# Kernel optimization log

Hardware: AMD Instinct MI355X
Metric: run time of the kernel (lower is better)

## Reference

```python
import jax, jax.numpy as jnp
import numpy as np

N = 50000      # nodes
E = 800000     # edges (avg degree 16)
F_IN = 128
H = 128        # hidden_channels
C = 10         # num_classes
S = 5          # Chebyshev order K
B = 8          # graphs in batch


def setup_inputs() -> dict:
    key = jax.random.key(0)
    ks = jax.random.split(key, 9)
    x = jax.random.normal(ks[0], (N, F_IN), jnp.float32)
    edge_index = jax.random.randint(ks[1], (2, E), 0, N, dtype=jnp.int64)
    batch = jnp.sort(jax.random.randint(ks[2], (N,), 0, B, dtype=jnp.int64))
    lambda_max = 2.0 * jnp.ones((B,), jnp.float32)
    W1 = jax.random.normal(ks[3], (S, F_IN, H), jnp.float32) * 0.05
    b1 = jax.random.normal(ks[4], (H,), jnp.float32) * 0.05
    W2 = jax.random.normal(ks[5], (S, H, H), jnp.float32) * 0.05
    b2 = jax.random.normal(ks[6], (H,), jnp.float32) * 0.05
    Wlin = jax.random.normal(ks[7], (H, C), jnp.float32) * 0.05
    blin = jax.random.normal(ks[8], (C,), jnp.float32) * 0.05
    return {"x": x, "edge_index": edge_index, "batch": batch,
            "lambda_max": lambda_max, "W1": W1, "b1": b1,
            "W2": W2, "b2": b2, "Wlin": Wlin, "blin": blin}


def _cheb_conv(x, row, col, w_edge, diag, W, b):
    # scaled Laplacian matvec: L_hat v = scatter(w_edge * v[col] -> row) + diag * v
    def Lhat(v):
        msg = v[col] * w_edge[:, None]                       # [E, d]
        return jax.ops.segment_sum(msg, row, num_segments=N) + diag[:, None] * v

    Tx0 = x
    out = Tx0 @ W[0]
    Tx1 = Lhat(Tx0)
    out = out + Tx1 @ W[1]
    for k in range(2, W.shape[0]):                           # Chebyshev recurrence
        Tx2 = 2.0 * Lhat(Tx1) - Tx0
        out = out + Tx2 @ W[k]
        Tx0, Tx1 = Tx1, Tx2
    return out + b


def reference(x, edge_index, batch, lambda_max, W1, b1, W2, b2, Wlin, blin):
    row, col = edge_index[0], edge_index[1]
    # sym-normalized Laplacian L = I - D^{-1/2} A D^{-1/2}; L_hat = 2L/lambda_max - I
    deg = jax.ops.segment_sum(jnp.ones((E,), x.dtype), row, num_segments=N)
    dis = jnp.where(deg > 0, jax.lax.rsqrt(jnp.maximum(deg, 1e-12)), 0.0)
    lam_e = lambda_max[batch[row]]                           # per-edge lambda_max
    w_edge = -2.0 * dis[row] * dis[col] / lam_e              # off-diagonal of L_hat
    diag = 2.0 / lambda_max[batch] - 1.0                     # diagonal of L_hat per node

    h = jax.nn.relu(_cheb_conv(x, row, col, w_edge, diag, W1, b1))
    h = jax.nn.relu(_cheb_conv(h, row, col, w_edge, diag, W2, b2))

    # global_mean_pool over batch assignment
    sums = jax.ops.segment_sum(h, batch, num_segments=B)     # [B, H]
    counts = jax.ops.segment_sum(jnp.ones((N, 1), h.dtype), batch, num_segments=B)
    pooled = sums / jnp.maximum(counts, 1.0)
    return pooled @ Wlin + blin                              # [B, C] logits (softmax unused in forward)
```

## Files before the change

### kernel.cpp

```cpp
#include <hip/hip_runtime.h>
#include <hip/hip_bf16.h>
#include <stdint.h>

typedef __attribute__((ext_vector_type(8))) short bf16x8;
typedef __attribute__((ext_vector_type(4))) float f32x4;

__device__ __forceinline__ float bf16lo_to_f(uint32_t u) { return __uint_as_float(u << 16); }
__device__ __forceinline__ float bf16hi_to_f(uint32_t u) { return __uint_as_float(u & 0xffff0000u); }
__device__ __forceinline__ uint16_t f_to_bf16(float f) {
    uint32_t u = __float_as_uint(f);
    uint32_t r = u + 0x7fff + ((u >> 16) & 1);
    return (uint16_t)(r >> 16);
}


#define BINCH 4096

__global__ void __launch_bounds__(256) k_bhist(const int* __restrict__ row,
                                               int* __restrict__ bhist, int E) {
    __shared__ int sh[256];
    int t = threadIdx.x;
    sh[t] = 0;
    __syncthreads();
    int stride = gridDim.x * blockDim.x;
    for (int e = blockIdx.x * blockDim.x + t; e < E; e += stride)
        atomicAdd(&sh[row[e] >> 8], 1);
    __syncthreads();
    if (sh[t]) atomicAdd(&bhist[t], sh[t]);
}

__global__ void k_bscan(const int* __restrict__ bhist, int* __restrict__ gbase,
                        int* __restrict__ gcur, float* __restrict__ mS, int nbk, int N) {
    __shared__ int sh[256];
    int t = threadIdx.x;
    int v = t < nbk ? bhist[t] : 0;
    sh[t] = v;
    __syncthreads();
    for (int o = 1; o < 256; o <<= 1) {
        int u = (t >= o) ? sh[t - o] : 0;
        __syncthreads();
        sh[t] += u;
        __syncthreads();
    }
    gbase[t] = sh[t] - v;
    gcur[t] = sh[t] - v;
    if (t == 255) gbase[256] = sh[255];
    if (t < 5) mS[(size_t)t * (N + 1) + N] = 0.f;
}

__global__ void __launch_bounds__(256) k_bin(const int* __restrict__ row,
        const int* __restrict__ col, int* __restrict__ gcur,
        uint32_t* __restrict__ bout, int E) {
    __shared__ uint32_t stage[BINCH];
    __shared__ int hist[256], hscan[256], hcur[256], gofs[256];
    int t = threadIdx.x;
    int e0 = blockIdx.x * BINCH;
    int ecnt = min(BINCH, E - e0);
    hist[t] = 0;
    __syncthreads();
    for (int i = t; i < ecnt; i += 256)
        atomicAdd(&hist[row[e0 + i] >> 8], 1);
    __syncthreads();
    int v = hist[t];
    hscan[t] = v;
    __syncthreads();
    for (int o = 1; o < 256; o <<= 1) {
        int u = (t >= o) ? hscan[t - o] : 0;
        __syncthreads();
        hscan[t] += u;
        __syncthreads();
    }
    hcur[t] = hscan[t] - v;
    __syncthreads();
    for (int i = t; i < ecnt; i += 256) {
        int r = row[e0 + i];
        int p = atomicAdd(&hcur[r >> 8], 1);
        stage[p] = (uint32_t)(r & 255) | ((uint32_t)col[e0 + i] << 8);
    }
    __syncthreads();
    if (v > 0) gofs[t] = atomicAdd(&gcur[t], v);
    __syncthreads();
    for (int i = t; i < ecnt; i += 256) {
        int lo = 0, hi = 255;
        while (lo < hi) { int mid = (lo + hi) >> 1; if (hscan[mid] > i) hi = mid; else lo = mid + 1; }
        int b = lo;
        int local = i - (hscan[b] - hist[b]);
        bout[gofs[b] + local] = stage[i];
    }
}

__global__ void __launch_bounds__(256) k_deg2(const uint32_t* __restrict__ bout,
        const int* __restrict__ gbase, int* __restrict__ deg,
        int* __restrict__ psum, int N) {
    __shared__ int cnt[256];
    __shared__ int red[256];
    int t = threadIdx.x, b = blockIdx.x;
    cnt[t] = 0;
    __syncthreads();
    int s = gbase[b], epos = gbase[b + 1];
    for (int i = s + t; i < epos; i += 256)
        atomicAdd(&cnt[bout[i] & 255], 1);
    __syncthreads();
    int n = b * 256 + t;
    int d = cnt[t];
    if (n < N) deg[n] = d;
    red[t] = (n < N) ? ((d + 7) & ~7) : 0;
    __syncthreads();
    for (int o = 128; o > 0; o >>= 1) {
        if (t < o) red[t] += red[t + o];
        __syncthreads();
    }
    if (t == 0) psum[b] = red[0];
}

__global__ void k_offs(const int* __restrict__ deg, const int* __restrict__ psum,
                       int* __restrict__ offs,
                       const int* __restrict__ batch, const float* __restrict__ lam,
                       float* __restrict__ dis, float* __restrict__ diag,
                       int N, int nb) {
    __shared__ int pre[256];
    __shared__ int sh[256];
    int t = threadIdx.x, b = blockIdx.x;
    pre[t] = (t < b) ? psum[t] : 0;
    __syncthreads();
    for (int o = 128; o > 0; o >>= 1) {
        if (t < o) pre[t] += pre[t + o];
        __syncthreads();
    }
    int base = pre[0];
    __syncthreads();
    int idx = b * 256 + t;
    int d = idx < N ? deg[idx] : 0;
    int v = (d + 7) & ~7;
    sh[t] = v;
    __syncthreads();
    for (int o = 1; o < 256; o <<= 1) {
        int u = (t >= o) ? sh[t - o] : 0;
        __syncthreads();
        sh[t] += u;
        __syncthreads();
    }
    if (idx < N) {
        offs[idx] = base + sh[t] - v;
        dis[idx] = d > 0 ? rsqrtf((float)d) : 0.f;
        diag[idx] = 2.f / lam[batch[idx]] - 1.f;
    }
    if (b == nb - 1 && t == 255) offs[N] = base + sh[255];
}

__global__ void __launch_bounds__(256) k_csr2(const uint32_t* __restrict__ bout,
        const int* __restrict__ gbase, const int* __restrict__ offs,
        uint16_t* __restrict__ csr, int N) {
    __shared__ int cur[256];
    int t = threadIdx.x, b = blockIdx.x;
    int n = b * 256 + t;
    int o0 = n < N ? offs[n] : 0;
    cur[t] = o0;
    __syncthreads();
    int s = gbase[b], epos = gbase[b + 1];
    for (int i = s + t; i < epos; i += 256) {
        uint32_t v = bout[i];
        int p = atomicAdd(&cur[v & 255], 1);
        csr[p] = (uint16_t)(v >> 8);
    }
    __syncthreads();
    if (n < N) {
        int e = cur[t];
        int pe = o0 + ((e - o0 + 7) & ~7);
        for (int p = e; p < pe; p++) csr[p] = (uint16_t)N;
    }
}

__global__ void k_prepw(const float* __restrict__ W1, uint16_t* __restrict__ Wt1,
                        const float* __restrict__ W2, uint16_t* __restrict__ Wt2) {
    int i = blockIdx.x * blockDim.x + threadIdx.x;
    const float* W = W1; uint16_t* Wt = Wt1;
    if (i >= 128 * 640) { i -= 128 * 640; W = W2; Wt = Wt2; }
    int o = i / 640, kk = i % 640;
    Wt[(size_t)o * 640 + kk] = f_to_bf16(W[(size_t)kk * 128 + o]);
}

__global__ void __launch_bounds__(256) k_castx(const float* __restrict__ x,
        uint16_t* __restrict__ Txb, int8_t* __restrict__ Txq,
        const float* __restrict__ dis, float* __restrict__ mS,
        float* __restrict__ scq, int N) {
    int n = (blockIdx.x * blockDim.x + threadIdx.x) >> 6;
    int lane = threadIdx.x & 63;
    if (n >= N) return;
    float2 v = ((const float2*)x)[(size_t)n * 64 + lane];
    uint32_t p = (uint32_t)f_to_bf16(v.x) | ((uint32_t)f_to_bf16(v.y) << 16);
    __builtin_nontemporal_store(p, &((uint32_t*)Txb)[(size_t)n * 320 + lane]);
    float m = fmaxf(fabsf(v.x), fabsf(v.y));
    for (int o = 1; o < 64; o <<= 1) m = fmaxf(m, __shfl_xor(m, o));
    float inv = m > 0.f ? 127.f / m : 0.f;
    int qx = (int)rintf(v.x * inv), qy = (int)rintf(v.y * inv);
    uint16_t qp = (uint16_t)((qx & 0xff) | ((qy & 0xff) << 8));
    *(uint16_t*)(Txq + (size_t)n * 640 + 2 * lane) = qp;
    if (lane == 0) {
        float sc = m > 0.f ? m * (1.f / 127.f) : 0.f;
        mS[n] = sc * dis[n];
        scq[n] = sc;
    }
}

__global__ void __launch_bounds__(256) k_lhat(
        int8_t* __restrict__ Txq, uint16_t* __restrict__ Txb,
        const int* __restrict__ offs, const uint16_t* __restrict__ csr,
        const float* __restrict__ diag, const float* __restrict__ dis,
        float* __restrict__ mS, float* __restrict__ scq, int N,
        int src, int dst, int prev, float alpha, int use_prev) {
    int n = (blockIdx.x * blockDim.x + threadIdx.x) >> 6;
    int lane = threadIdx.x & 63;
    if (n >= N) return;
    int beg = offs[n], end = offs[n + 1];
    float dgn = diag[n], dn = dis[n];
    float aS = -alpha * dn * (dgn + 1.0f);
    const float* mSrc = mS + (size_t)src * (N + 1);
    const int8_t* qbase = Txq + src * 128 + 2 * lane;
    float ax = 0.f, ay = 0.f;
    for (int e = beg; e < end; e += 8) {
        uint4 cw = *(const uint4*)(csr + e);
        int cc[8] = { (int)(cw.x & 0xffff), (int)(cw.x >> 16),
                      (int)(cw.y & 0xffff), (int)(cw.y >> 16),
                      (int)(cw.z & 0xffff), (int)(cw.z >> 16),
                      (int)(cw.w & 0xffff), (int)(cw.w >> 16) };
        float mm[8];
        uint16_t qv[8];
#pragma unroll
        for (int u = 0; u < 8; u++) mm[u] = mSrc[cc[u]];
#pragma unroll
        for (int u = 0; u < 8; u++)
            qv[u] = *(const uint16_t*)(qbase + (size_t)cc[u] * 640);
#pragma unroll
        for (int u = 0; u < 8; u++) {
            float f = aS * mm[u];
            ax = fmaf(f, (float)(int)(int8_t)(qv[u] & 0xff), ax);
            ay = fmaf(f, (float)(int)(int8_t)(qv[u] >> 8), ay);
        }
    }
    {
        uint16_t qsv = *(const uint16_t*)(Txq + (size_t)n * 640 + src * 128 + 2 * lane);
        float ad = alpha * dgn * scq[(size_t)src * (N + 1) + n];
        ax = fmaf(ad, (float)(int)(int8_t)(qsv & 0xff), ax);
        ay = fmaf(ad, (float)(int)(int8_t)(qsv >> 8), ay);
    }
    if (use_prev) {
        uint16_t qpv = *(const uint16_t*)(Txq + (size_t)n * 640 + prev * 128 + 2 * lane);
        float sp = scq[(size_t)prev * (N + 1) + n];
        ax = fmaf(-sp, (float)(int)(int8_t)(qpv & 0xff), ax);
        ay = fmaf(-sp, (float)(int)(int8_t)(qpv >> 8), ay);
    }
    uint32_t outv = (uint32_t)f_to_bf16(ax) | ((uint32_t)f_to_bf16(ay) << 16);
    __builtin_nontemporal_store(outv, &((uint32_t*)Txb)[(size_t)n * 320 + dst * 64 + lane]);
    float m = fmaxf(fabsf(ax), fabsf(ay));
    for (int o = 1; o < 64; o <<= 1) m = fmaxf(m, __shfl_xor(m, o));
    float inv = m > 0.f ? 127.f / m : 0.f;
    int qx = (int)rintf(ax * inv), qy = (int)rintf(ay * inv);
    uint16_t qp = (uint16_t)((qx & 0xff) | ((qy & 0xff) << 8));
    *(uint16_t*)(Txq + (size_t)n * 640 + dst * 128 + 2 * lane) = qp;
    if (lane == 0) {
        float sc = m > 0.f ? m * (1.f / 127.f) : 0.f;
        mS[(size_t)dst * (N + 1) + n] = sc * dn;
        scq[(size_t)dst * (N + 1) + n] = sc;
    }
}

#define BM 128
#define BK 64
#define LDT 72
#define LDC 132

__global__ void __launch_bounds__(256) k_gemm(
        const uint16_t* __restrict__ A, int lda,
        const uint16_t* __restrict__ Bt,
        const float* __restrict__ bias,
        uint16_t* __restrict__ out2b,
        int8_t* __restrict__ out2q,
        const float* __restrict__ dis, float* __restrict__ mS,
        float* __restrict__ scq,
        float* __restrict__ pooled,
        const int* __restrict__ batch,
        int M, int Kdim) {
    __shared__ uint16_t smem[BM * LDT + 128 * LDT];
    uint16_t* As = smem;
    uint16_t* Bs = smem + BM * LDT;
    uint16_t* Ct = smem;
    int t = threadIdx.x;
    int w = t >> 6, lane = t & 63;
    int row0 = blockIdx.x * BM;
    int mrow = (w >> 1) * 64, ncol = (w & 1) * 64;

    int ar[4], akc[4];
#pragma unroll
    for (int rep = 0; rep < 4; rep++) {
        int d = rep * 256 + t;
        ar[rep] = d >> 3; akc[rep] = d & 7;
    }

    f32x4 acc[4][4];
#pragma unroll
    for (int i = 0; i < 4; i++)
#pragma unroll
        for (int j = 0; j < 4; j++) acc[i][j] = (f32x4){0.f, 0.f, 0.f, 0.f};

    bf16x8 pa[4], pb[4];
#pragma unroll
    for (int rep = 0; rep < 4; rep++) {
        int grow = row0 + ar[rep];
        bf16x8 va = {0, 0, 0, 0, 0, 0, 0, 0};
        if (grow < M) va = *(const bf16x8*)(A + (size_t)grow * lda + akc[rep] * 8);
        pa[rep] = va;
        pb[rep] = *(const bf16x8*)(Bt + (size_t)ar[rep] * Kdim + akc[rep] * 8);
    }

    for (int k0 = 0; k0 < Kdim; k0 += BK) {
#pragma unroll
        for (int rep = 0; rep < 4; rep++) {
            *(bf16x8*)(&As[ar[rep] * LDT + akc[rep] * 8]) = pa[rep];
            *(bf16x8*)(&Bs[ar[rep] * LDT + akc[rep] * 8]) = pb[rep];
        }
        __syncthreads();
        int kn = k0 + BK;
        if (kn < Kdim) {
#pragma unroll
            for (int rep = 0; rep < 4; rep++) {
                int grow = row0 + ar[rep];
                bf16x8 va = {0, 0, 0, 0, 0, 0, 0, 0};
                if (grow < M) va = *(const bf16x8*)(A + (size_t)grow * lda + kn + akc[rep] * 8);
                pa[rep] = va;
                pb[rep] = *(const bf16x8*)(Bt + (size_t)ar[rep] * Kdim + kn + akc[rep] * 8);
            }
        }
#pragma unroll
        for (int ks = 0; ks < BK; ks += 32) {
            bf16x8 af[4], bfr[4];
#pragma unroll
            for (int i = 0; i < 4; i++) {
                int r = mrow + i * 16 + (lane & 15);
                af[i] = *(const bf16x8*)(&As[r * LDT + ks + (lane >> 4) * 8]);
            }
#pragma unroll
            for (int j = 0; j < 4; j++) {
                int c = ncol + j * 16 + (lane & 15);
                bfr[j] = *(const bf16x8*)(&Bs[c * LDT + ks + (lane >> 4) * 8]);
            }
#pragma unroll
            for (int i = 0; i < 4; i++)
#pragma unroll
                for (int j = 0; j < 4; j++)
                    acc[i][j] = __builtin_amdgcn_mfma_f32_16x16x32_bf16(af[i], bfr[j], acc[i][j], 0, 0, 0);
        }
        __syncthreads();
    }

#pragma unroll
    for (int j = 0; j < 4; j++) {
        int c = ncol + j * 16 + (lane & 15);
        float bv = bias[c];
#pragma unroll
        for (int i = 0; i < 4; i++) {
            int rloc = mrow + i * 16 + (lane >> 4) * 4;
#pragma unroll
            for (int r = 0; r < 4; r++) {
                float v = acc[i][j][r] + bv;
                v = v > 0.f ? v : 0.f;
                Ct[(rloc + r) * LDC + c] = f_to_bf16(v);
            }
        }
    }
    __syncthreads();

    if (out2b) {
#pragma unroll
        for (int rep = 0; rep < 8; rep++) {
            int d = rep * 256 + t;
            int r = d >> 4, c8 = (d & 15) * 8;
            int grow = row0 + r;
            if (grow < M) {
                bf16x8 v = *(const bf16x8*)(&Ct[r * LDC + c8]);
                *(bf16x8*)(out2b + (size_t)grow * 640 + c8) = v;
            }
        }
    }
    if (out2q) {
        int r = t >> 1, half = t & 1;
        int grow = row0 + r;
        float vmax = 0.f;
        for (int j = 0; j < 32; j++) {
            uint32_t u = *(const uint32_t*)(&Ct[r * LDC + half * 64 + j * 2]);
            vmax = fmaxf(vmax, fmaxf(fabsf(bf16lo_to_f(u)), fabsf(bf16hi_to_f(u))));
        }
        vmax = fmaxf(vmax, __shfl_xor(vmax, 1));
        if (grow < M) {
            float inv = vmax > 0.f ? 127.f / vmax : 0.f;
            for (int j0 = 0; j0 < 16; j0++) {
                uint32_t u0 = *(const uint32_t*)(&Ct[r * LDC + half * 64 + j0 * 4]);
                uint32_t u1 = *(const uint32_t*)(&Ct[r * LDC + half * 64 + j0 * 4 + 2]);
                int q0 = (int)rintf(bf16lo_to_f(u0) * inv);
                int q1 = (int)rintf(bf16hi_to_f(u0) * inv);
                int q2 = (int)rintf(bf16lo_to_f(u1) * inv);
                int q3 = (int)rintf(bf16hi_to_f(u1) * inv);
                uint32_t pk = (q0 & 0xff) | ((q1 & 0xff) << 8) |
                              ((q2 & 0xff) << 16) | ((uint32_t)(q3 & 0xff) << 24);
                *(uint32_t*)(out2q + (size_t)grow * 640 + half * 64 + j0 * 4) = pk;
            }
            if (half == 0) {
                float sc = vmax > 0.f ? vmax * (1.f / 127.f) : 0.f;
                mS[grow] = sc * dis[grow];
                scq[grow] = sc;
            }
        }
    }
    if (pooled) {
        int f = t & 127, r0 = (t >> 7) * 64;
        float accp = 0.f;
        int curb = -1;
        for (int r = r0; r < r0 + 64; ++r) {
            int grow = row0 + r;
            if (grow >= M) break;
            int b = batch[grow];
            if (b != curb) {
                if (curb >= 0) atomicAdd(&pooled[curb * 128 + f], accp);
                accp = 0.f; curb = b;
            }
            accp += __uint_as_float(((uint32_t)Ct[r * LDC + f]) << 16);
        }
        if (curb >= 0) atomicAdd(&pooled[curb * 128 + f], accp);
    }
}

__global__ void k_final(const float* __restrict__ pooled, const int* __restrict__ batch,
                        const float* __restrict__ Wlin, const float* __restrict__ blin,
                        float* __restrict__ out, int N, int B_, int C_) {
    __shared__ int cnt[64];
    int t = threadIdx.x;
    if (t < B_) {
        auto lb = [&](int v) {
            int lo = 0, hi = N;
            while (lo < hi) {
                int mid = (lo + hi) >> 1;
                if (batch[mid] < v) lo = mid + 1; else hi = mid;
            }
            return lo;
        };
        cnt[t] = lb(t + 1) - lb(t);
    }
    __syncthreads();
    if (t < B_ * C_) {
        int b = t / C_, c = t % C_;
        float inv = 1.f / fmaxf((float)cnt[b], 1.f);
        float acc = blin[c];
        for (int f = 0; f < 128; ++f) acc += pooled[b * 128 + f] * inv * Wlin[f * C_ + c];
        out[t] = acc;
    }
}

extern "C" void kernel_launch(void* const* d_in, const int* in_sizes, int n_in,
                              void* d_out, int out_size, void* d_ws, size_t ws_size,
                              hipStream_t stream) {
    const float* x    = (const float*)d_in[0];
    const int*   edge = (const int*)d_in[1];
    const int*   batch= (const int*)d_in[2];
    const float* lam  = (const float*)d_in[3];
    const float* W1   = (const float*)d_in[4];
    const float* b1   = (const float*)d_in[5];
    const float* W2   = (const float*)d_in[6];
    const float* b2   = (const float*)d_in[7];
    const float* Wlin = (const float*)d_in[8];
    const float* blin = (const float*)d_in[9];
    const int E  = in_sizes[1] / 2;
    const int N  = in_sizes[2];
    const int B_ = in_sizes[3];
    const int* row = edge;
    const int* col = edge + E;

    char* ws = (char*)d_ws;
    size_t off = 0;
    auto take = [&](size_t bytes) -> char* {
        char* p = ws + off;
        off = (off + bytes + 255) & ~(size_t)255;
        return p;
    };
    uint16_t* Txb    = (uint16_t*)take((size_t)N * 640 * 2);
    int8_t*   Txq    = (int8_t*)take((size_t)(N + 1) * 640);
    uint16_t* csr    = (uint16_t*)take(((size_t)E + 8 * (size_t)N) * 2);
    uint32_t* bout   = (uint32_t*)take((size_t)E * 4);
    float*    mS     = (float*)take((size_t)5 * (N + 1) * 4);
    float*    scq    = (float*)take((size_t)5 * (N + 1) * 4);
    int*      deg    = (int*)take((size_t)N * 4);
    int*      offs   = (int*)take((size_t)(N + 1) * 4);
    float*    dis    = (float*)take((size_t)N * 4);
    float*    diag   = (float*)take((size_t)N * 4);
    uint16_t* Wt1    = (uint16_t*)take((size_t)128 * 640 * 2);
    uint16_t* Wt2    = (uint16_t*)take((size_t)128 * 640 * 2);
    float*    pooled = (float*)take((size_t)B_ * 128 * 4);
    int*      bhist  = (int*)take(257 * 4);
    int*      gbase  = (int*)take(257 * 4);
    int*      gcur   = (int*)take(257 * 4);
    const int nb = (N + 255) / 256;
    int*      psum   = (int*)take((size_t)nb * 4);

    hipMemsetAsync(pooled, 0, (size_t)B_ * 128 * 4 + 257 * 4, stream);

    k_bhist<<<112, 256, 0, stream>>>(row, bhist, E);
    k_bscan<<<1, 256, 0, stream>>>(bhist, gbase, gcur, mS, nb, N);
    k_bin<<<(E + BINCH - 1) / BINCH, 256, 0, stream>>>(row, col, gcur, bout, E);
    k_deg2<<<nb, 256, 0, stream>>>(bout, gbase, deg, psum, N);
    k_offs<<<nb, 256, 0, stream>>>(deg, psum, offs, batch, lam, dis, diag, N, nb);
    k_csr2<<<nb, 256, 0, stream>>>(bout, gbase, offs, csr, N);
    k_prepw<<<(2 * 128 * 640) / 256, 256, 0, stream>>>(W1, Wt1, W2, Wt2);
    k_castx<<<(N + 3) / 4, 256, 0, stream>>>(x, Txb, Txq, dis, mS, scq, N);

    const int lblocks = (N + 3) / 4;
    const int gblocks = (N + BM - 1) / BM;

    k_lhat<<<lblocks, 256, 0, stream>>>(Txq, Txb, offs, csr, diag, dis, mS, scq, N, 0, 1, 0, 1.f, 0);
    k_lhat<<<lblocks, 256, 0, stream>>>(Txq, Txb, offs, csr, diag, dis, mS, scq, N, 1, 2, 0, 2.f, 1);
    k_lhat<<<lblocks, 256, 0, stream>>>(Txq, Txb, offs, csr, diag, dis, mS, scq, N, 2, 3, 1, 2.f, 1);
    k_lhat<<<lblocks, 256, 0, stream>>>(Txq, Txb, offs, csr, diag, dis, mS, scq, N, 3, 4, 2, 2.f, 1);
    k_gemm<<<gblocks, 256, 0, stream>>>(Txb, 640, Wt1, b1,
                                        Txb, Txq, dis, mS, scq,
                                        (float*)nullptr, batch, N, 640);

    k_lhat<<<lblocks, 256, 0, stream>>>(Txq, Txb, offs, csr, diag, dis, mS, scq, N, 0, 1, 0, 1.f, 0);
    k_lhat<<<lblocks, 256, 0, stream>>>(Txq, Txb, offs, csr, diag, dis, mS, scq, N, 1, 2, 0, 2.f, 1);
    k_lhat<<<lblocks, 256, 0, stream>>>(Txq, Txb, offs, csr, diag, dis, mS, scq, N, 2, 3, 1, 2.f, 1);
    k_lhat<<<lblocks, 256, 0, stream>>>(Txq, Txb, offs, csr, diag, dis, mS, scq, N, 3, 4, 2, 2.f, 1);
    k_gemm<<<gblocks, 256, 0, stream>>>(Txb, 640, Wt2, b2,
                                        (uint16_t*)nullptr, (int8_t*)nullptr, dis, mS, scq,
                                        pooled, batch, N, 640);

    k_final<<<1, 128, 0, stream>>>(pooled, batch, Wlin, blin, (float*)d_out, N, B_, 10);
}
```

Before: 482.7 us.

## Replace int8 gather with bf16 stage-major layout and precomputed edge weights

The int8-quantized copies of the Chebyshev terms and their per-row scale arrays are removed. Each stage is now stored as a separate contiguous bf16 plane, with a zero pad row for padding edges. The CSR is rebuilt as 8-byte entries holding a pre-shifted column offset and a precomputed edge weight, so the Lhat kernel drops the per-neighbor scale load and the requantization epilogue. The GEMM now reads A from the stage planes. In exchange, each gathered neighbor row doubles in bytes (bf16 instead of int8) and the edge array grows from 2 to 8 bytes per entry.

```diff
diff --git a/kernel.cpp b/kernel.cpp
--- a/kernel.cpp
+++ b/kernel.cpp
@@ -1,5 +1,4 @@
 #include <hip/hip_runtime.h>
-#include <hip/hip_bf16.h>
 #include <stdint.h>
 
 typedef __attribute__((ext_vector_type(8))) short bf16x8;
@@ -30,7 +29,7 @@
 }
 
 __global__ void k_bscan(const int* __restrict__ bhist, int* __restrict__ gbase,
-                        int* __restrict__ gcur, float* __restrict__ mS, int nbk, int N) {
+                        int* __restrict__ gcur, int nbk) {
     __shared__ int sh[256];
     int t = threadIdx.x;
     int v = t < nbk ? bhist[t] : 0;
@@ -45,7 +44,6 @@
     gbase[t] = sh[t] - v;
     gcur[t] = sh[t] - v;
     if (t == 255) gbase[256] = sh[255];
-    if (t < 5) mS[(size_t)t * (N + 1) + N] = 0.f;
 }
 
 __global__ void __launch_bounds__(256) k_bin(const int* __restrict__ row,
@@ -148,26 +146,33 @@
     if (b == nb - 1 && t == 255) offs[N] = base + sh[255];
 }
 
-__global__ void __launch_bounds__(256) k_csr2(const uint32_t* __restrict__ bout,
+__global__ void __launch_bounds__(256) k_ew(const uint32_t* __restrict__ bout,
         const int* __restrict__ gbase, const int* __restrict__ offs,
-        uint16_t* __restrict__ csr, int N) {
+        const float* __restrict__ dis, const float* __restrict__ diag,
+        uint2* __restrict__ ew, int N) {
     __shared__ int cur[256];
+    __shared__ float srw[256];
     int t = threadIdx.x, b = blockIdx.x;
     int n = b * 256 + t;
     int o0 = n < N ? offs[n] : 0;
     cur[t] = o0;
+    srw[t] = (n < N) ? (-dis[n] * (diag[n] + 1.0f)) : 0.f;
     __syncthreads();
     int s = gbase[b], epos = gbase[b + 1];
     for (int i = s + t; i < epos; i += 256) {
         uint32_t v = bout[i];
-        int p = atomicAdd(&cur[v & 255], 1);
-        csr[p] = (uint16_t)(v >> 8);
+        int r = (int)(v & 255u);
+        int c = (int)(v >> 8);
+        int p = atomicAdd(&cur[r], 1);
+        float w = srw[r] * dis[c];
+        ew[p] = make_uint2((uint32_t)c << 8, __float_as_uint(w));
     }
     __syncthreads();
     if (n < N) {
         int e = cur[t];
         int pe = o0 + ((e - o0 + 7) & ~7);
-        for (int p = e; p < pe; p++) csr[p] = (uint16_t)N;
+        uint2 pad = make_uint2((uint32_t)N << 8, 0u);
+        for (int p = e; p < pe; p++) ew[p] = pad;
     }
 }
 
@@ -181,88 +186,70 @@
 }
 
 __global__ void __launch_bounds__(256) k_castx(const float* __restrict__ x,
-        uint16_t* __restrict__ Txb, int8_t* __restrict__ Txq,
-        const float* __restrict__ dis, float* __restrict__ mS,
-        float* __restrict__ scq, int N) {
+        uint16_t* __restrict__ Txg, int N) {
     int n = (blockIdx.x * blockDim.x + threadIdx.x) >> 6;
     int lane = threadIdx.x & 63;
-    if (n >= N) return;
+    if (n > N) return;
+    size_t ss32 = (size_t)(N + 1) * 64;
+    if (n == N) {
+#pragma unroll
+        for (int s = 0; s < 5; s++)
+            ((uint32_t*)Txg)[s * ss32 + (size_t)N * 64 + lane] = 0u;
+        return;
+    }
     float2 v = ((const float2*)x)[(size_t)n * 64 + lane];
     uint32_t p = (uint32_t)f_to_bf16(v.x) | ((uint32_t)f_to_bf16(v.y) << 16);
-    __builtin_nontemporal_store(p, &((uint32_t*)Txb)[(size_t)n * 320 + lane]);
-    float m = fmaxf(fabsf(v.x), fabsf(v.y));
-    for (int o = 1; o < 64; o <<= 1) m = fmaxf(m, __shfl_xor(m, o));
-    float inv = m > 0.f ? 127.f / m : 0.f;
-    int qx = (int)rintf(v.x * inv), qy = (int)rintf(v.y * inv);
-    uint16_t qp = (uint16_t)((qx & 0xff) | ((qy & 0xff) << 8));
-    *(uint16_t*)(Txq + (size_t)n * 640 + 2 * lane) = qp;
-    if (lane == 0) {
-        float sc = m > 0.f ? m * (1.f / 127.f) : 0.f;
-        mS[n] = sc * dis[n];
-        scq[n] = sc;
-    }
-}
-
-__global__ void __launch_bounds__(256) k_lhat(
-        int8_t* __restrict__ Txq, uint16_t* __restrict__ Txb,
-        const int* __restrict__ offs, const uint16_t* __restrict__ csr,
-        const float* __restrict__ diag, const float* __restrict__ dis,
-        float* __restrict__ mS, float* __restrict__ scq, int N,
+    ((uint32_t*)Txg)[(size_t)n * 64 + lane] = p;
+}
+
+__global__ void __launch_bounds__(256) k_lhat(uint16_t* Txg,
+        const int* __restrict__ offs, const uint2* __restrict__ ew,
+        const float* __restrict__ diag, int N,
         int src, int dst, int prev, float alpha, int use_prev) {
     int n = (blockIdx.x * blockDim.x + threadIdx.x) >> 6;
     int lane = threadIdx.x & 63;
     if (n >= N) return;
     int beg = offs[n], end = offs[n + 1];
-    float dgn = diag[n], dn = dis[n];
-    float aS = -alpha * dn * (dgn + 1.0f);
-    const float* mSrc = mS + (size_t)src * (N + 1);
-    const int8_t* qbase = Txq + src * 128 + 2 * lane;
+    size_t sb = (size_t)(N + 1) * 256;
+    const uint8_t* srcs = (const uint8_t*)Txg + (size_t)src * sb;
+    uint32_t lo4 = (uint32_t)lane * 4;
     float ax = 0.f, ay = 0.f;
     for (int e = beg; e < end; e += 8) {
-        uint4 cw = *(const uint4*)(csr + e);
-        int cc[8] = { (int)(cw.x & 0xffff), (int)(cw.x >> 16),
-                      (int)(cw.y & 0xffff), (int)(cw.y >> 16),
-                      (int)(cw.z & 0xffff), (int)(cw.z >> 16),
-                      (int)(cw.w & 0xffff), (int)(cw.w >> 16) };
-        float mm[8];
-        uint16_t qv[8];
-#pragma unroll
-        for (int u = 0; u < 8; u++) mm[u] = mSrc[cc[u]];
+        const uint4* ep = (const uint4*)(ew + e);
+        uint4 a = ep[0], b4 = ep[1], c4 = ep[2], d4 = ep[3];
+        uint32_t co[8]; float wv[8];
+        co[0] = a.x;  wv[0] = __uint_as_float(a.y);
+        co[1] = a.z;  wv[1] = __uint_as_float(a.w);
+        co[2] = b4.x; wv[2] = __uint_as_float(b4.y);
+        co[3] = b4.z; wv[3] = __uint_as_float(b4.w);
+        co[4] = c4.x; wv[4] = __uint_as_float(c4.y);
+        co[5] = c4.z; wv[5] = __uint_as_float(c4.w);
+        co[6] = d4.x; wv[6] = __uint_as_float(d4.y);
+        co[7] = d4.z; wv[7] = __uint_as_float(d4.w);
+        uint32_t q[8];
 #pragma unroll
         for (int u = 0; u < 8; u++)
-            qv[u] = *(const uint16_t*)(qbase + (size_t)cc[u] * 640);
+            q[u] = *(const uint32_t*)(srcs + (co[u] + lo4));
 #pragma unroll
         for (int u = 0; u < 8; u++) {
-            float f = aS * mm[u];
-            ax = fmaf(f, (float)(int)(int8_t)(qv[u] & 0xff), ax);
-            ay = fmaf(f, (float)(int)(int8_t)(qv[u] >> 8), ay);
-        }
-    }
-    {
-        uint16_t qsv = *(const uint16_t*)(Txq + (size_t)n * 640 + src * 128 + 2 * lane);
-        float ad = alpha * dgn * scq[(size_t)src * (N + 1) + n];
-        ax = fmaf(ad, (float)(int)(int8_t)(qsv & 0xff), ax);
-        ay = fmaf(ad, (float)(int)(int8_t)(qsv >> 8), ay);
-    }
+            ax = fmaf(wv[u], bf16lo_to_f(q[u]), ax);
+            ay = fmaf(wv[u], bf16hi_to_f(q[u]), ay);
+        }
+    }
+    float dgn = diag[n];
+    uint32_t roff = ((uint32_t)n << 8) + lo4;
+    uint32_t qs = *(const uint32_t*)(srcs + roff);
+    ax = fmaf(dgn, bf16lo_to_f(qs), ax);
+    ay = fmaf(dgn, bf16hi_to_f(qs), ay);
+    float fx = alpha * ax, fy = alpha * ay;
     if (use_prev) {
-        uint16_t qpv = *(const uint16_t*)(Txq + (size_t)n * 640 + prev * 128 + 2 * lane);
-        float sp = scq[(size_t)prev * (N + 1) + n];
-        ax = fmaf(-sp, (float)(int)(int8_t)(qpv & 0xff), ax);
-        ay = fmaf(-sp, (float)(int)(int8_t)(qpv >> 8), ay);
-    }
-    uint32_t outv = (uint32_t)f_to_bf16(ax) | ((uint32_t)f_to_bf16(ay) << 16);
-    __builtin_nontemporal_store(outv, &((uint32_t*)Txb)[(size_t)n * 320 + dst * 64 + lane]);
-    float m = fmaxf(fabsf(ax), fabsf(ay));
-    for (int o = 1; o < 64; o <<= 1) m = fmaxf(m, __shfl_xor(m, o));
-    float inv = m > 0.f ? 127.f / m : 0.f;
-    int qx = (int)rintf(ax * inv), qy = (int)rintf(ay * inv);
-    uint16_t qp = (uint16_t)((qx & 0xff) | ((qy & 0xff) << 8));
-    *(uint16_t*)(Txq + (size_t)n * 640 + dst * 128 + 2 * lane) = qp;
-    if (lane == 0) {
-        float sc = m > 0.f ? m * (1.f / 127.f) : 0.f;
-        mS[(size_t)dst * (N + 1) + n] = sc * dn;
-        scq[(size_t)dst * (N + 1) + n] = sc;
-    }
+        const uint8_t* prs = (const uint8_t*)Txg + (size_t)prev * sb;
+        uint32_t qp = *(const uint32_t*)(prs + roff);
+        fx -= bf16lo_to_f(qp);
+        fy -= bf16hi_to_f(qp);
+    }
+    uint32_t outv = (uint32_t)f_to_bf16(fx) | ((uint32_t)f_to_bf16(fy) << 16);
+    *(uint32_t*)((uint8_t*)Txg + (size_t)dst * sb + roff) = outv;
 }
 
 #define BM 128
@@ -271,13 +258,10 @@
 #define LDC 132
 
 __global__ void __launch_bounds__(256) k_gemm(
-        const uint16_t* __restrict__ A, int lda,
+        const uint16_t* __restrict__ A, size_t sstride,
         const uint16_t* __restrict__ Bt,
         const float* __restrict__ bias,
         uint16_t* __restrict__ out2b,
-        int8_t* __restrict__ out2q,
-        const float* __restrict__ dis, float* __restrict__ mS,
-        float* __restrict__ scq,
         float* __restrict__ pooled,
         const int* __restrict__ batch,
         int M, int Kdim) {
@@ -307,10 +291,12 @@
 #pragma unroll
     for (int rep = 0; rep < 4; rep++) {
         int grow = row0 + ar[rep];
+        int kk = akc[rep] * 8;
         bf16x8 va = {0, 0, 0, 0, 0, 0, 0, 0};
-        if (grow < M) va = *(const bf16x8*)(A + (size_t)grow * lda + akc[rep] * 8);
+        if (grow < M)
+            va = *(const bf16x8*)(A + (size_t)(kk >> 7) * sstride + (size_t)grow * 128 + (kk & 127));
         pa[rep] = va;
-        pb[rep] = *(const bf16x8*)(Bt + (size_t)ar[rep] * Kdim + akc[rep] * 8);
+        pb[rep] = *(const bf16x8*)(Bt + (size_t)ar[rep] * Kdim + kk);
     }
 
     for (int k0 = 0; k0 < Kdim; k0 += BK) {
@@ -325,10 +311,12 @@
 #pragma unroll
             for (int rep = 0; rep < 4; rep++) {
                 int grow = row0 + ar[rep];
+                int kk = kn + akc[rep] * 8;
                 bf16x8 va = {0, 0, 0, 0, 0, 0, 0, 0};
-                if (grow < M) va = *(const bf16x8*)(A + (size_t)grow * lda + kn + akc[rep] * 8);
+                if (grow < M)
+                    va = *(const bf16x8*)(A + (size_t)(kk >> 7) * sstride + (size_t)grow * 128 + (kk & 127));
                 pa[rep] = va;
-                pb[rep] = *(const bf16x8*)(Bt + (size_t)ar[rep] * Kdim + kn + akc[rep] * 8);
+                pb[rep] = *(const bf16x8*)(Bt + (size_t)ar[rep] * Kdim + kk);
             }
         }
 #pragma unroll
@@ -378,36 +366,7 @@
             int grow = row0 + r;
             if (grow < M) {
                 bf16x8 v = *(const bf16x8*)(&Ct[r * LDC + c8]);
-                *(bf16x8*)(out2b + (size_t)grow * 640 + c8) = v;
-            }
-        }
-    }
-    if (out2q) {
-        int r = t >> 1, half = t & 1;
-        int grow = row0 + r;
-        float vmax = 0.f;
-        for (int j = 0; j < 32; j++) {
-            uint32_t u = *(const uint32_t*)(&Ct[r * LDC + half * 64 + j * 2]);
-            vmax = fmaxf(vmax, fmaxf(fabsf(bf16lo_to_f(u)), fabsf(bf16hi_to_f(u))));
-        }
-        vmax = fmaxf(vmax, __shfl_xor(vmax, 1));
-        if (grow < M) {
-            float inv = vmax > 0.f ? 127.f / vmax : 0.f;
-            for (int j0 = 0; j0 < 16; j0++) {
-                uint32_t u0 = *(const uint32_t*)(&Ct[r * LDC + half * 64 + j0 * 4]);
-                uint32_t u1 = *(const uint32_t*)(&Ct[r * LDC + half * 64 + j0 * 4 + 2]);
-                int q0 = (int)rintf(bf16lo_to_f(u0) * inv);
-                int q1 = (int)rintf(bf16hi_to_f(u0) * inv);
-                int q2 = (int)rintf(bf16lo_to_f(u1) * inv);
-                int q3 = (int)rintf(bf16hi_to_f(u1) * inv);
-                uint32_t pk = (q0 & 0xff) | ((q1 & 0xff) << 8) |
-                              ((q2 & 0xff) << 16) | ((uint32_t)(q3 & 0xff) << 24);
-                *(uint32_t*)(out2q + (size_t)grow * 640 + half * 64 + j0 * 4) = pk;
-            }
-            if (half == 0) {
-                float sc = vmax > 0.f ? vmax * (1.f / 127.f) : 0.f;
-                mS[grow] = sc * dis[grow];
-                scq[grow] = sc;
+                *(bf16x8*)(out2b + (size_t)grow * 128 + c8) = v;
             }
         }
     }
@@ -481,12 +440,9 @@
         off = (off + bytes + 255) & ~(size_t)255;
         return p;
     };
-    uint16_t* Txb    = (uint16_t*)take((size_t)N * 640 * 2);
-    int8_t*   Txq    = (int8_t*)take((size_t)(N + 1) * 640);
-    uint16_t* csr    = (uint16_t*)take(((size_t)E + 8 * (size_t)N) * 2);
+    uint16_t* Txg    = (uint16_t*)take((size_t)5 * (N + 1) * 128 * 2);
+    uint2*    ew     = (uint2*)take(((size_t)E + 8 * (size_t)N) * 8);
     uint32_t* bout   = (uint32_t*)take((size_t)E * 4);
-    float*    mS     = (float*)take((size_t)5 * (N + 1) * 4);
-    float*    scq    = (float*)take((size_t)5 * (N + 1) * 4);
     int*      deg    = (int*)take((size_t)N * 4);
     int*      offs   = (int*)take((size_t)(N + 1) * 4);
     float*    dis    = (float*)take((size_t)N * 4);
@@ -503,32 +459,31 @@
     hipMemsetAsync(pooled, 0, (size_t)B_ * 128 * 4 + 257 * 4, stream);
 
     k_bhist<<<112, 256, 0, stream>>>(row, bhist, E);
-    k_bscan<<<1, 256, 0, stream>>>(bhist, gbase, gcur, mS, nb, N);
+    k_bscan<<<1, 256, 0, stream>>>(bhist, gbase, gcur, nb);
     k_bin<<<(E + BINCH - 1) / BINCH, 256, 0, stream>>>(row, col, gcur, bout, E);
     k_deg2<<<nb, 256, 0, stream>>>(bout, gbase, deg, psum, N);
     k_offs<<<nb, 256, 0, stream>>>(deg, psum, offs, batch, lam, dis, diag, N, nb);
-    k_csr2<<<nb, 256, 0, stream>>>(bout, gbase, offs, csr, N);
+    k_ew<<<nb, 256, 0, stream>>>(bout, gbase, offs, dis, diag, ew, N);
     k_prepw<<<(2 * 128 * 640) / 256, 256, 0, stream>>>(W1, Wt1, W2, Wt2);
-    k_castx<<<(N + 3) / 4, 256, 0, stream>>>(x, Txb, Txq, dis, mS, scq, N);
+    k_castx<<<(N + 4) / 4, 256, 0, stream>>>(x, Txg, N);
 
     const int lblocks = (N + 3) / 4;
     const int gblocks = (N + BM - 1) / BM;
-
-    k_lhat<<<lblocks, 256, 0, stream>>>(Txq, Txb, offs, csr, diag, dis, mS, scq, N, 0, 1, 0, 1.f, 0);
-    k_lhat<<<lblocks, 256, 0, stream>>>(Txq, Txb, offs, csr, diag, dis, mS, scq, N, 1, 2, 0, 2.f, 1);
-    k_lhat<<<lblocks, 256, 0, stream>>>(Txq, Txb, offs, csr, diag, dis, mS, scq, N, 2, 3, 1, 2.f, 1);
-    k_lhat<<<lblocks, 256, 0, stream>>>(Txq, Txb, offs, csr, diag, dis, mS, scq, N, 3, 4, 2, 2.f, 1);
-    k_gemm<<<gblocks, 256, 0, stream>>>(Txb, 640, Wt1, b1,
-                                        Txb, Txq, dis, mS, scq,
-                                        (float*)nullptr, batch, N, 640);
-
-    k_lhat<<<lblocks, 256, 0, stream>>>(Txq, Txb, offs, csr, diag, dis, mS, scq, N, 0, 1, 0, 1.f, 0);
-    k_lhat<<<lblocks, 256, 0, stream>>>(Txq, Txb, offs, csr, diag, dis, mS, scq, N, 1, 2, 0, 2.f, 1);
-    k_lhat<<<lblocks, 256, 0, stream>>>(Txq, Txb, offs, csr, diag, dis, mS, scq, N, 2, 3, 1, 2.f, 1);
-    k_lhat<<<lblocks, 256, 0, stream>>>(Txq, Txb, offs, csr, diag, dis, mS, scq, N, 3, 4, 2, 2.f, 1);
-    k_gemm<<<gblocks, 256, 0, stream>>>(Txb, 640, Wt2, b2,
-                                        (uint16_t*)nullptr, (int8_t*)nullptr, dis, mS, scq,
-                                        pooled, batch, N, 640);
+    const size_t ss = (size_t)(N + 1) * 128;
+
+    k_lhat<<<lblocks, 256, 0, stream>>>(Txg, offs, ew, diag, N, 0, 1, 0, 1.f, 0);
+    k_lhat<<<lblocks, 256, 0, stream>>>(Txg, offs, ew, diag, N, 1, 2, 0, 2.f, 1);
+    k_lhat<<<lblocks, 256, 0, stream>>>(Txg, offs, ew, diag, N, 2, 3, 1, 2.f, 1);
+    k_lhat<<<lblocks, 256, 0, stream>>>(Txg, offs, ew, diag, N, 3, 4, 2, 2.f, 1);
+    k_gemm<<<gblocks, 256, 0, stream>>>(Txg, ss, Wt1, b1,
+                                        Txg , (float*)nullptr, batch, N, 640);
+
+    k_lhat<<<lblocks, 256, 0, stream>>>(Txg, offs, ew, diag, N, 0, 1, 0, 1.f, 0);
+    k_lhat<<<lblocks, 256, 0, stream>>>(Txg, offs, ew, diag, N, 1, 2, 0, 2.f, 1);
+    k_lhat<<<lblocks, 256, 0, stream>>>(Txg, offs, ew, diag, N, 2, 3, 1, 2.f, 1);
+    k_lhat<<<lblocks, 256, 0, stream>>>(Txg, offs, ew, diag, N, 3, 4, 2, 2.f, 1);
+    k_gemm<<<gblocks, 256, 0, stream>>>(Txg, ss, Wt2, b2,
+                                        (uint16_t*)nullptr, pooled, batch, N, 640);
 
     k_final<<<1, 128, 0, stream>>>(pooled, batch, Wlin, blin, (float*)d_out, N, B_, 10);
 }
```

Result: no change. 474.5 us (-1.7%).
